# Performance work log

Hardware: AMD Instinct MI355X
Metric: run time of the kernel (lower is better)

## Reference

```python
import jax, jax.numpy as jnp
import numpy as np

EMB = 1024
HEADS = 16
HD = EMB // HEADS  # 64
FF = 4 * EMB
EPS = 1e-5


def _layernorm(x, g, b):
    mu = jnp.mean(x, axis=-1, keepdims=True)
    var = jnp.mean(jnp.square(x - mu), axis=-1, keepdims=True)
    return (x - mu) * jax.lax.rsqrt(var + EPS) * g + b


def setup_inputs() -> dict:
    key = jax.random.key(0)
    ks = jax.random.split(key, 12)
    s_in = 1.0 / np.sqrt(EMB)
    s_ff = 1.0 / np.sqrt(FF)
    return {
        "x": jax.random.normal(ks[0], (4, 2048, EMB), dtype=jnp.float32),
        # per-head projections stacked: [H, C, HD]
        "Wq": jax.random.normal(ks[1], (HEADS, EMB, HD), dtype=jnp.float32) * s_in,
        "Wk": jax.random.normal(ks[2], (HEADS, EMB, HD), dtype=jnp.float32) * s_in,
        "Wv": jax.random.normal(ks[3], (HEADS, EMB, HD), dtype=jnp.float32) * s_in,
        "Wo": jax.random.normal(ks[4], (EMB, EMB), dtype=jnp.float32) * s_in,
        "bo": jnp.zeros((EMB,), dtype=jnp.float32),
        "W1": jax.random.normal(ks[5], (EMB, FF), dtype=jnp.float32) * s_in,
        "b1": jnp.zeros((FF,), dtype=jnp.float32),
        "W2": jax.random.normal(ks[6], (FF, EMB), dtype=jnp.float32) * s_ff,
        "b2": jnp.zeros((EMB,), dtype=jnp.float32),
        "g1": jnp.ones((EMB,), dtype=jnp.float32),
        "be1": jnp.zeros((EMB,), dtype=jnp.float32),
        "g2": jnp.ones((EMB,), dtype=jnp.float32),
        "be2": jnp.zeros((EMB,), dtype=jnp.float32),
    }


def reference(x, Wq, Wk, Wv, Wo, bo, W1, b1, W2, b2, g1, be1, g2, be2):
    B, T, C = x.shape
    h = _layernorm(x, g1, be1)
    # per-head projections: [B,H,T,HD]
    q = jnp.einsum("btc,hcd->bhtd", h, Wq)
    k = jnp.einsum("btc,hcd->bhtd", h, Wk)
    v = jnp.einsum("btc,hcd->bhtd", h, Wv)
    scores = jnp.einsum("bhtd,bhsd->bhts", q, k) * (HD ** -0.5)
    causal = jnp.tril(jnp.ones((T, T), dtype=bool))
    scores = jnp.where(causal, scores, -jnp.inf)
    attn = jax.nn.softmax(scores, axis=-1)
    out = jnp.einsum("bhts,bhsd->bhtd", attn, v)
    out = out.transpose(0, 2, 1, 3).reshape(B, T, C)  # concat heads
    x = x + out @ Wo + bo
    h2 = _layernorm(x, g2, be2)
    x = x + jax.nn.relu(h2 @ W1 + b1) @ W2 + b2
    return x
```

## Files before the change

### kernel.cpp

```cpp
#include <hip/hip_runtime.h>

typedef unsigned short u16;
typedef unsigned int u32;
typedef float f32x4 __attribute__((ext_vector_type(4)));
typedef short s16x8 __attribute__((ext_vector_type(8)));
typedef u16 u16x4 __attribute__((ext_vector_type(4)));
typedef u32 u32x2 __attribute__((ext_vector_type(2)));
typedef u32 u32x4 __attribute__((ext_vector_type(4)));

#define DEVI static __device__ __forceinline__

DEVI u16 f2bf(float f) {
  u32 u = __float_as_uint(f);
  return (u16)((u + 0x7fffu + ((u >> 16) & 1u)) >> 16);
}

DEVI float fexp2(float x) {
#if __has_builtin(__builtin_amdgcn_exp2f)
  return __builtin_amdgcn_exp2f(x);
#else
  return __expf(x * 0.69314718056f);
#endif
}

DEVI void g2l16(const void* g, void* l) {
  __builtin_amdgcn_global_load_lds((const __attribute__((address_space(1))) u32*)g,
                                   (__attribute__((address_space(3))) u32*)l,
                                   16, 0, 0);
}

__global__ __launch_bounds__(256) void trans_w(
    const float* __restrict__ src, u16* __restrict__ dst, int R, int C)
{
  __shared__ __attribute__((aligned(16))) u16 tile[64 * 65];
  const int t = threadIdx.x;
  const int c0 = blockIdx.x * 64, r0 = blockIdx.y * 64;
#pragma unroll
  for (int i = 0; i < 16; ++i) {
    const int idx = i * 256 + t;
    const int c = idx & 63, r = idx >> 6;
    tile[c * 65 + r] = f2bf(src[(long)(r0 + r) * C + c0 + c]);
  }
  __syncthreads();
#pragma unroll
  for (int i = 0; i < 16; ++i) {
    const int idx = i * 256 + t;
    const int r = idx & 63, c = idx >> 6;
    dst[(long)(c0 + c) * R + r0 + r] = tile[c * 65 + r];
  }
}

__global__ __launch_bounds__(256) void trans_qkvw(
    const float* __restrict__ Wq, const float* __restrict__ Wk,
    const float* __restrict__ Wv, u16* __restrict__ dst)
{
  __shared__ __attribute__((aligned(16))) u16 tile[64 * 65];
  const int t = threadIdx.x;
  const int c0 = blockIdx.x * 64;
  const int mh = blockIdx.y;
  const int mat = mh >> 4, h = mh & 15;
  const float* src = (mat == 0 ? Wq : (mat == 1 ? Wk : Wv)) + (long)h * 65536;
#pragma unroll
  for (int i = 0; i < 16; ++i) {
    const int idx = i * 256 + t;
    const int d = idx & 63, c = idx >> 6;
    tile[d * 65 + c] = f2bf(src[(long)(c0 + c) * 64 + d]);
  }
  __syncthreads();
  const long nb = (long)(mat * 1024 + h * 64);
#pragma unroll
  for (int i = 0; i < 16; ++i) {
    const int idx = i * 256 + t;
    const int d = idx >> 6, c = idx & 63;
    dst[(nb + d) * 1024 + c0 + c] = tile[d * 65 + c];
  }
}

__global__ __launch_bounds__(256) void vtrans(
    const u16* __restrict__ qkv, u16* __restrict__ vtg)
{
  __shared__ __attribute__((aligned(16))) u32 tile[64 * 33];
  const int t = threadIdx.x;
  const int tt = blockIdx.x, bh = blockIdx.y;
  const long bt0 = (long)(bh >> 4) * 2048;
  const int h = bh & 15;
  const int t0 = tt * 64;
  const int r2 = t >> 3, c8 = t & 7;
  const u16* src = qkv + (bt0 + t0 + 2 * r2) * 3072 + 2048 + h * 64 + c8 * 8;
  const s16x8 a = *(const s16x8*)src;
  const s16x8 b = *(const s16x8*)(src + 3072);
#pragma unroll
  for (int j = 0; j < 8; ++j)
    tile[(c8 * 8 + j) * 33 + r2] = (u32)(u16)a[j] | ((u32)(u16)b[j] << 16);
  __syncthreads();
#pragma unroll
  for (int it = 0; it < 2; ++it) {
    const int idx = it * 256 + t;
    const int d = idx >> 3, g = idx & 7;
    u32 p0 = tile[d * 33 + g];
    u32 p1 = tile[d * 33 + g + 8];
    u32 p2 = tile[d * 33 + g + 16];
    u32 p3 = tile[d * 33 + g + 24];
    u32x4 w;
    w[0] = (p0 & 0xffffu) | (p1 << 16);
    w[1] = (p2 & 0xffffu) | (p3 << 16);
    w[2] = (p0 >> 16) | (p1 & 0xffff0000u);
    w[3] = (p2 >> 16) | (p3 & 0xffff0000u);
    *(u32x4*)(vtg + (long)bh * 131072 + (long)d * 2048 + t0 + g * 8) = w;
  }
}

__global__ __launch_bounds__(256) void ln_kernel(
    const float* __restrict__ x, const float* __restrict__ g,
    const float* __restrict__ be, u16* __restrict__ out)
{
  const int t = threadIdx.x, wv = t >> 6, l = t & 63;
  const long row = (long)blockIdx.x * 4 + wv;
  const float* xr = x + row * 1024;
  f32x4 v[4];
#pragma unroll
  for (int i = 0; i < 4; ++i) v[i] = *(const f32x4*)(xr + i * 256 + l * 4);
  float s = 0.f, sq = 0.f;
#pragma unroll
  for (int i = 0; i < 4; ++i)
#pragma unroll
    for (int j = 0; j < 4; ++j) { s += v[i][j]; sq += v[i][j] * v[i][j]; }
#pragma unroll
  for (int mask = 1; mask < 64; mask <<= 1) {
    s  += __shfl_xor(s, mask);
    sq += __shfl_xor(sq, mask);
  }
  const float mean = s * (1.f / 1024.f);
  const float var  = sq * (1.f / 1024.f) - mean * mean;
  const float rs = rsqrtf(var + 1e-5f);
#pragma unroll
  for (int i = 0; i < 4; ++i) {
    f32x4 gv = *(const f32x4*)(g  + i * 256 + l * 4);
    f32x4 bv = *(const f32x4*)(be + i * 256 + l * 4);
    u16x4 o;
#pragma unroll
    for (int j = 0; j < 4; ++j) o[j] = f2bf((v[i][j] - mean) * rs * gv[j] + bv[j]);
    *(u16x4*)(out + row * 1024 + i * 256 + l * 4) = o;
  }
}

template <typename OutT, bool RELU, bool BIAS, bool RESID>
__global__ __launch_bounds__(256) void gemm_bt(
    const u16* __restrict__ A, const u16* __restrict__ Bt,
    OutT* __restrict__ Cout, const float* __restrict__ bias,
    const float* __restrict__ resid, int M, int N, int K)
{
  __shared__ __attribute__((aligned(16))) u16 As[2][8192];
  __shared__ __attribute__((aligned(16))) u16 Bs[2][8192];
  const int t  = threadIdx.x;
  const int l  = t & 63;
  const int wv = t >> 6;
  const int lr = l & 15, lg = l >> 4;
  const int wr = wv >> 1, wc = wv & 1;
  const long m0 = (long)blockIdx.x * 128, n0 = (long)blockIdx.y * 128;

  f32x4 acc[4][4] = {};

  const int srow8 = t >> 3;
  const int swc = ((t & 7) ^ (srow8 & 7)) << 3;
  const u16* Ap = A  + (m0 + srow8) * K + swc;
  const u16* Bp = Bt + (n0 + srow8) * K + swc;

#define GSTAGE(buf, kof)                                                      \
  {                                                                           \
    _Pragma("unroll")                                                         \
    for (int i = 0; i < 4; ++i) {                                             \
      g2l16(Ap + (long)i * 32 * K + (kof), (char*)As[buf] + (i * 256 + t) * 16); \
      g2l16(Bp + (long)i * 32 * K + (kof), (char*)Bs[buf] + (i * 256 + t) * 16); \
    }                                                                         \
  }

#define GCOMPUTE(buf)                                                         \
  {                                                                           \
    const char* Ab = (const char*)As[buf];                                    \
    const char* Bb = (const char*)Bs[buf];                                    \
    _Pragma("unroll")                                                         \
    for (int kk = 0; kk < 2; ++kk) {                                          \
      s16x8 af[4], bfr[4];                                                    \
      _Pragma("unroll")                                                       \
      for (int m = 0; m < 4; ++m) {                                           \
        const int row = wr * 64 + m * 16 + lr;                                \
        af[m] = *(const s16x8*)(Ab + row * 128 +                              \
                                ((((kk * 4 + lg) << 4) ^ ((row & 7) << 4)))); \
      }                                                                       \
      _Pragma("unroll")                                                       \
      for (int n = 0; n < 4; ++n) {                                           \
        const int row = wc * 64 + n * 16 + lr;                                \
        bfr[n] = *(const s16x8*)(Bb + row * 128 +                             \
                                 ((((kk * 4 + lg) << 4) ^ ((row & 7) << 4))));\
      }                                                                       \
      _Pragma("unroll")                                                       \
      for (int m = 0; m < 4; ++m)                                             \
        _Pragma("unroll")                                                     \
        for (int n = 0; n < 4; ++n)                                           \
          acc[m][n] = __builtin_amdgcn_mfma_f32_16x16x32_bf16(af[m], bfr[n],  \
                                                              acc[m][n], 0, 0, 0); \
    }                                                                         \
  }

  const int nt = K >> 6;
  GSTAGE(0, 0);
  __syncthreads();
  int cur = 0;
  for (int tt = 0; tt < nt - 1; ++tt) {
    GSTAGE(cur ^ 1, (tt + 1) * 64);
    GCOMPUTE(cur);
    __syncthreads();
    cur ^= 1;
  }
  GCOMPUTE(cur);
#undef GSTAGE
#undef GCOMPUTE

  float bv[4];
#pragma unroll
  for (int n = 0; n < 4; ++n)
    bv[n] = BIAS ? bias[n0 + wc * 64 + n * 16 + lr] : 0.f;

#pragma unroll
  for (int m = 0; m < 4; ++m) {
#pragma unroll
    for (int i = 0; i < 4; ++i) {
      const long row = m0 + wr * 64 + m * 16 + lg * 4 + i;
#pragma unroll
      for (int n = 0; n < 4; ++n) {
        const long col = n0 + wc * 64 + n * 16 + lr;
        float v = acc[m][n][i] + bv[n];
        if (RESID) v += resid[row * N + col];
        if (RELU)  v = fmaxf(v, 0.f);
        if constexpr (sizeof(OutT) == 2) Cout[row * N + col] = f2bf(v);
        else                             Cout[row * N + col] = v;
      }
    }
  }
}

__global__ __launch_bounds__(256) void attn_kernel(
    const u16* __restrict__ qkv, const u16* __restrict__ vtg,
    u16* __restrict__ out)
{
  __shared__ __attribute__((aligned(16))) u16 Kl[4096];
  __shared__ __attribute__((aligned(16))) u16 Vl[4096];
  __shared__ __attribute__((aligned(16))) u16 Pl[4][1024];

  const float c2 = 0.18033688011112042f;

  const int t  = threadIdx.x;
  const int wv = t >> 6, l = t & 63;
  const int lr = l & 15, lg = l >> 4;
  const int bh = blockIdx.y;
  const long bt0 = (long)(bh >> 4) * 2048;
  const int h = bh & 15;

  const int r0 = t >> 3, c8 = t & 7;
  const int swc = (c8 ^ (r0 & 7)) << 3;
  const u16* ksrc = qkv + (bt0 + r0) * 3072 + 1024 + h * 64 + swc;
  const u16* vsrc = vtg + (long)bh * 131072 + (long)r0 * 2048 + swc;
  char* kd = (char*)Kl + t * 16;
  char* vd = (char*)Vl + t * 16;
  char* pw = (char*)Pl + wv * 2048;

#pragma unroll
  for (int half = 0; half < 2; ++half) {
    const int qte = half ? (31 - (int)blockIdx.x) : (int)blockIdx.x;
    const int qrow0 = qte * 64 + wv * 16;

    s16x8 aq[2];
#pragma unroll
    for (int dc = 0; dc < 2; ++dc)
      aq[dc] = *(const s16x8*)(qkv + (bt0 + qrow0 + lr) * 3072 + h * 64 + dc * 32 + lg * 8);

    f32x4 O[4] = {};
    float mi[4], li[4];
#pragma unroll
    for (int i = 0; i < 4; ++i) { mi[i] = -__builtin_inff(); li[i] = 0.f; }

    for (int scn = 0; scn <= qte; ++scn) {
      const int s0 = scn * 64;
      __syncthreads();
      g2l16(ksrc + (long)s0 * 3072,        kd);
      g2l16(ksrc + (long)(s0 + 32) * 3072, kd + 4096);
      g2l16(vsrc + s0,                     vd);
      g2l16(vsrc + s0 + 65536,             vd + 4096);
      __syncthreads();

      s16x8 kf[4][2];
#pragma unroll
      for (int n = 0; n < 4; ++n) {
        const int row = n * 16 + lr;
        const int sw = (row & 7) << 4;
#pragma unroll
        for (int dh = 0; dh < 2; ++dh)
          kf[n][dh] = *(const s16x8*)((const char*)Kl + row * 128 +
                                      (((dh * 4 + lg) << 4) ^ sw));
      }

      f32x4 S[4];
#pragma unroll
      for (int n = 0; n < 4; ++n) {
        f32x4 z = {};
        z = __builtin_amdgcn_mfma_f32_16x16x32_bf16(aq[0], kf[n][0], z, 0, 0, 0);
        S[n] = __builtin_amdgcn_mfma_f32_16x16x32_bf16(aq[1], kf[n][1], z, 0, 0, 0);
      }

      float mt[4];
      if (scn == qte) {
#pragma unroll
        for (int i = 0; i < 4; ++i) {
          const int qg = qrow0 + lg * 4 + i;
#pragma unroll
          for (int n = 0; n < 4; ++n)
            S[n][i] = (s0 + n * 16 + lr <= qg) ? S[n][i] : -__builtin_inff();
          mt[i] = fmaxf(fmaxf(S[0][i], S[1][i]), fmaxf(S[2][i], S[3][i]));
        }
      } else {
#pragma unroll
        for (int i = 0; i < 4; ++i)
          mt[i] = fmaxf(fmaxf(S[0][i], S[1][i]), fmaxf(S[2][i], S[3][i]));
      }
#pragma unroll
      for (int msk = 1; msk < 16; msk <<= 1)
#pragma unroll
        for (int i = 0; i < 4; ++i)
          mt[i] = fmaxf(mt[i], __shfl_xor(mt[i], msk));

      const int grow = (mt[0] > mi[0]) | (mt[1] > mi[1]) |
                       (mt[2] > mi[2]) | (mt[3] > mi[3]);
      if (__any(grow)) {
#pragma unroll
        for (int i = 0; i < 4; ++i) {
          const float mn = fmaxf(mi[i], mt[i]);
          const float so = fexp2((mi[i] - mn) * c2);
          mi[i] = mn;
          li[i] *= so;
#pragma unroll
          for (int n = 0; n < 4; ++n) O[n][i] *= so;
        }
      }

#pragma unroll
      for (int i = 0; i < 4; ++i) {
        const float nmc = -mi[i] * c2;
        float p[4];
#pragma unroll
        for (int n = 0; n < 4; ++n) p[n] = fexp2(fmaf(S[n][i], c2, nmc));
        li[i] += (p[0] + p[1]) + (p[2] + p[3]);
        const int q_l = lg * 4 + i;
        u32x2 pk;
        pk[0] = (u32)f2bf(p[0]) | ((u32)f2bf(p[1]) << 16);
        pk[1] = (u32)f2bf(p[2]) | ((u32)f2bf(p[3]) << 16);
        *(u32x2*)(pw + q_l * 128 + ((((lr >> 1) << 4) ^ ((q_l & 7) << 4)) + ((lr & 1) << 3))) = pk;
      }

      s16x8 vf[4][2];
#pragma unroll
      for (int dn = 0; dn < 4; ++dn) {
        const int row = dn * 16 + lr;
        const int sw = (row & 7) << 4;
#pragma unroll
        for (int kk = 0; kk < 2; ++kk)
          vf[dn][kk] = *(const s16x8*)((const char*)Vl + row * 128 +
                                       (((kk * 4 + lg) << 4) ^ sw));
      }
      s16x8 pa[2];
#pragma unroll
      for (int kk = 0; kk < 2; ++kk)
        pa[kk] = *(const s16x8*)(pw + lr * 128 + (((kk * 4 + lg) << 4) ^ ((lr & 7) << 4)));
#pragma unroll
      for (int dn = 0; dn < 4; ++dn) {
        O[dn] = __builtin_amdgcn_mfma_f32_16x16x32_bf16(pa[0], vf[dn][0], O[dn], 0, 0, 0);
        O[dn] = __builtin_amdgcn_mfma_f32_16x16x32_bf16(pa[1], vf[dn][1], O[dn], 0, 0, 0);
      }
    }

#pragma unroll
    for (int msk = 1; msk < 16; msk <<= 1)
#pragma unroll
      for (int i = 0; i < 4; ++i)
        li[i] += __shfl_xor(li[i], msk);

#pragma unroll
    for (int i = 0; i < 4; ++i) {
      const float rl = 1.f / li[i];
      const long ob = (bt0 + qrow0 + lg * 4 + i) * 1024 + h * 64 + lr;
#pragma unroll
      for (int n = 0; n < 4; ++n)
        out[ob + n * 16] = f2bf(O[n][i] * rl);
    }
  }
}

extern "C" void kernel_launch(void* const* d_in, const int* in_sizes, int n_in,
                              void* d_out, int out_size, void* d_ws, size_t ws_size,
                              hipStream_t stream)
{
  const float* x   = (const float*)d_in[0];
  const float* Wq  = (const float*)d_in[1];
  const float* Wk  = (const float*)d_in[2];
  const float* Wv  = (const float*)d_in[3];
  const float* Wo  = (const float*)d_in[4];
  const float* bo  = (const float*)d_in[5];
  const float* W1  = (const float*)d_in[6];
  const float* b1  = (const float*)d_in[7];
  const float* W2  = (const float*)d_in[8];
  const float* b2  = (const float*)d_in[9];
  const float* g1  = (const float*)d_in[10];
  const float* be1 = (const float*)d_in[11];
  const float* g2  = (const float*)d_in[12];
  const float* be2 = (const float*)d_in[13];
  float* outp = (float*)d_out;

  char* ws = (char*)d_ws;
  u16*   qkvT = (u16*)ws;
  u16*   woT  = (u16*)(ws + 6291456);
  u16*   w1T  = (u16*)(ws + 8388608);
  u16*   w2T  = (u16*)(ws + 16777216);
  float* x2   = (float*)(ws + 25165824);
  u16*   attno= (u16*)(ws + 58720256);
  u16*   h2   = (u16*)(ws + 75497472);
  u16*   hbf  = (u16*)(ws + 92274688);
  u16*   vtg  = (u16*)(ws + 92274688);
  u16*   qkvb = (u16*)(ws + 109051904);
  u16*   ffn1 = (u16*)(ws + 92274688);
  (void)in_sizes; (void)n_in; (void)out_size; (void)ws_size;

  trans_qkvw<<<dim3(16, 48), 256, 0, stream>>>(Wq, Wk, Wv, qkvT);
  trans_w<<<dim3(16, 16), 256, 0, stream>>>(Wo, woT, 1024, 1024);
  trans_w<<<dim3(64, 16), 256, 0, stream>>>(W1, w1T, 1024, 4096);
  trans_w<<<dim3(16, 64), 256, 0, stream>>>(W2, w2T, 4096, 1024);

  ln_kernel<<<2048, 256, 0, stream>>>(x, g1, be1, hbf);
  gemm_bt<u16, false, false, false><<<dim3(64, 24), 256, 0, stream>>>(
      hbf, qkvT, qkvb, nullptr, nullptr, 8192, 3072, 1024);
  vtrans<<<dim3(32, 64), 256, 0, stream>>>(qkvb, vtg);
  attn_kernel<<<dim3(16, 64), 256, 0, stream>>>(qkvb, vtg, attno);
  gemm_bt<float, false, true, true><<<dim3(64, 8), 256, 0, stream>>>(
      attno, woT, x2, bo, x, 8192, 1024, 1024);
  ln_kernel<<<2048, 256, 0, stream>>>(x2, g2, be2, h2);
  gemm_bt<u16, true, true, false><<<dim3(64, 32), 256, 0, stream>>>(
      h2, w1T, ffn1, b1, nullptr, 8192, 4096, 1024);
  gemm_bt<float, false, true, true><<<dim3(64, 8), 256, 0, stream>>>(
      ffn1, w2T, outp, b2, x2, 8192, 1024, 4096);
}
```

Baseline: 517.1 us.

## Double-buffer K/V tiles in attention and remap blocks per XCD

The attention kernel now keeps two LDS buffers for K and V. The next tile's global-to-LDS copy is issued before computing on the current tile, which drops one barrier per iteration and overlaps loads with MFMA work. The launch is flattened to a 1D grid, and block IDs are remapped so that the 16 query tiles of the same batch-head group land on the same XCD, which is meant to improve L2 reuse of K/V. The cost is more LDS per block, which may lower occupancy, and correctness depends on g2l16 completing before the next barrier.

```diff
diff --git a/kernel.cpp b/kernel.cpp
--- a/kernel.cpp
+++ b/kernel.cpp
@@ -244,8 +244,8 @@
     const u16* __restrict__ qkv, const u16* __restrict__ vtg,
     u16* __restrict__ out)
 {
-  __shared__ __attribute__((aligned(16))) u16 Kl[4096];
-  __shared__ __attribute__((aligned(16))) u16 Vl[4096];
+  __shared__ __attribute__((aligned(16))) u16 Kl[2][4096];
+  __shared__ __attribute__((aligned(16))) u16 Vl[2][4096];
   __shared__ __attribute__((aligned(16))) u16 Pl[4][1024];
 
   const float c2 = 0.18033688011112042f;
@@ -253,7 +253,10 @@
   const int t  = threadIdx.x;
   const int wv = t >> 6, l = t & 63;
   const int lr = l & 15, lg = l >> 4;
-  const int bh = blockIdx.y;
+  const int lid = (int)blockIdx.x;
+  const int xcd = lid & 7, ii = lid >> 3;
+  const int bh = xcd * 8 + (ii >> 4);
+  const int qt = ii & 15;
   const long bt0 = (long)(bh >> 4) * 2048;
   const int h = bh & 15;
 
@@ -261,13 +264,19 @@
   const int swc = (c8 ^ (r0 & 7)) << 3;
   const u16* ksrc = qkv + (bt0 + r0) * 3072 + 1024 + h * 64 + swc;
   const u16* vsrc = vtg + (long)bh * 131072 + (long)r0 * 2048 + swc;
-  char* kd = (char*)Kl + t * 16;
-  char* vd = (char*)Vl + t * 16;
   char* pw = (char*)Pl + wv * 2048;
 
+#define ASTAGE(buf, s0)                                                \
+  {                                                                    \
+    g2l16(ksrc + (long)(s0) * 3072,        (char*)Kl[buf] + t * 16);   \
+    g2l16(ksrc + (long)((s0) + 32) * 3072, (char*)Kl[buf] + 4096 + t * 16); \
+    g2l16(vsrc + (s0),                     (char*)Vl[buf] + t * 16);   \
+    g2l16(vsrc + (s0) + 65536,             (char*)Vl[buf] + 4096 + t * 16); \
+  }
+
 #pragma unroll
   for (int half = 0; half < 2; ++half) {
-    const int qte = half ? (31 - (int)blockIdx.x) : (int)blockIdx.x;
+    const int qte = half ? (31 - qt) : qt;
     const int qrow0 = qte * 64 + wv * 16;
 
     s16x8 aq[2];
@@ -280,14 +289,17 @@
 #pragma unroll
     for (int i = 0; i < 4; ++i) { mi[i] = -__builtin_inff(); li[i] = 0.f; }
 
+    __syncthreads();
+    ASTAGE(0, 0);
+    int cur = 0;
+
     for (int scn = 0; scn <= qte; ++scn) {
+      __syncthreads();
+      if (scn < qte) ASTAGE(cur ^ 1, (scn + 1) * 64);
+
       const int s0 = scn * 64;
-      __syncthreads();
-      g2l16(ksrc + (long)s0 * 3072,        kd);
-      g2l16(ksrc + (long)(s0 + 32) * 3072, kd + 4096);
-      g2l16(vsrc + s0,                     vd);
-      g2l16(vsrc + s0 + 65536,             vd + 4096);
-      __syncthreads();
+      const char* Kb = (const char*)Kl[cur];
+      const char* Vb = (const char*)Vl[cur];
 
       s16x8 kf[4][2];
 #pragma unroll
@@ -296,8 +308,7 @@
         const int sw = (row & 7) << 4;
 #pragma unroll
         for (int dh = 0; dh < 2; ++dh)
-          kf[n][dh] = *(const s16x8*)((const char*)Kl + row * 128 +
-                                      (((dh * 4 + lg) << 4) ^ sw));
+          kf[n][dh] = *(const s16x8*)(Kb + row * 128 + (((dh * 4 + lg) << 4) ^ sw));
       }
 
       f32x4 S[4];
@@ -364,8 +375,7 @@
         const int sw = (row & 7) << 4;
 #pragma unroll
         for (int kk = 0; kk < 2; ++kk)
-          vf[dn][kk] = *(const s16x8*)((const char*)Vl + row * 128 +
-                                       (((kk * 4 + lg) << 4) ^ sw));
+          vf[dn][kk] = *(const s16x8*)(Vb + row * 128 + (((kk * 4 + lg) << 4) ^ sw));
       }
       s16x8 pa[2];
 #pragma unroll
@@ -376,6 +386,7 @@
         O[dn] = __builtin_amdgcn_mfma_f32_16x16x32_bf16(pa[0], vf[dn][0], O[dn], 0, 0, 0);
         O[dn] = __builtin_amdgcn_mfma_f32_16x16x32_bf16(pa[1], vf[dn][1], O[dn], 0, 0, 0);
       }
+      cur ^= 1;
     }
 
 #pragma unroll
@@ -393,6 +404,7 @@
         out[ob + n * 16] = f2bf(O[n][i] * rl);
     }
   }
+#undef ASTAGE
 }
 
 extern "C" void kernel_launch(void* const* d_in, const int* in_sizes, int n_in,
@@ -438,7 +450,7 @@
   gemm_bt<u16, false, false, false><<<dim3(64, 24), 256, 0, stream>>>(
       hbf, qkvT, qkvb, nullptr, nullptr, 8192, 3072, 1024);
   vtrans<<<dim3(32, 64), 256, 0, stream>>>(qkvb, vtg);
-  attn_kernel<<<dim3(16, 64), 256, 0, stream>>>(qkvb, vtg, attno);
+  attn_kernel<<<1024, 256, 0, stream>>>(qkvb, vtg, attno);
   gemm_bt<float, false, true, true><<<dim3(64, 8), 256, 0, stream>>>(
       attno, woT, x2, bo, x, 8192, 1024, 1024);
   ln_kernel<<<2048, 256, 0, stream>>>(x2, g2, be2, h2);
```

Result: no change. 517.1 us (-0.0%).
